# Kernel optimization log

Measured on AMD Instinct MI355X. Metric: run time of the kernel, lower is better.

The kernel has to match this reference:

```python
import jax, jax.numpy as jnp
import numpy as np

BLOCK = 100  # hard-coded block size in the original module


def setup_inputs() -> dict:
    key = jax.random.key(0)
    k1, k2 = jax.random.split(key)
    N_freqs = 128
    n = N_freqs * BLOCK  # 12800
    # DPP kernel: symmetric PD so every 100x100 diagonal block has positive logdet
    R = jax.random.normal(k1, (n, n), dtype=jnp.float32) * 0.05
    L_kernel = (R + R.T) * 0.5 + 2.0 * jnp.eye(n, dtype=jnp.float32)
    weights = jax.random.normal(k2, (n,), dtype=jnp.float32)
    return {"weights": weights, "L_kernel": L_kernel, "N_freqs": N_freqs}


def reference(weights, L_kernel, N_freqs):
    # Gather the N_freqs diagonal 100x100 blocks without touching off-diagonals
    blocks4 = L_kernel.reshape(N_freqs, BLOCK, N_freqs, BLOCK)
    idx = jnp.arange(N_freqs)
    diag_blocks = blocks4[idx, :, idx, :]  # [N_freqs, 100, 100]
    s = jax.nn.sigmoid(weights).reshape(N_freqs, BLOCK)  # [N_freqs, 100]
    I = jnp.eye(BLOCK, dtype=L_kernel.dtype)
    # diag(s_i) @ (B_i - I) + I, batched over blocks
    M = s[:, :, None] * (diag_blocks - I) + I  # [N_freqs, 100, 100]
    sign, logabs = jnp.linalg.slogdet(M)
    # torch.logdet returns nan for non-positive determinant
    logdets = jnp.where(sign > 0, logabs, jnp.nan)
    within_freq_dets = jnp.sum(logdets)
    within_freq_dets_tensor = logdets.astype(jnp.float32)
    return (within_freq_dets, within_freq_dets_tensor)
```

## Files before the change

### kernel.cpp

```cpp
#include <hip/hip_runtime.h>
#include <math.h>

#define BLK 100
#define NF  128
#define NTOT (NF * BLK)
#define P   104
#define NT  512

__device__ __forceinline__ float4 fnma4(float4 v, float s, const float4 p) {
    v.x -= s * p.x; v.y -= s * p.y; v.z -= s * p.z; v.w -= s * p.w; return v;
}
__device__ __forceinline__ float4 mul4(float4 v, float s) {
    v.x *= s; v.y *= s; v.z *= s; v.w *= s; return v;
}
__device__ __forceinline__ float rdl(float x, int l) {
    return __uint_as_float(__builtin_amdgcn_readlane(__float_as_uint(x), l));
}
__device__ __forceinline__ float4 swap32(float4 v) {
    float4 o;
    o.x = __shfl_xor(v.x, 32); o.y = __shfl_xor(v.y, 32);
    o.z = __shfl_xor(v.z, 32); o.w = __shfl_xor(v.w, 32);
    return o;
}

#define LD4(r, c4) (*reinterpret_cast<float4*>(&a[(r) * P + 4 * (c4)]))

#define PANEL_CORE()                                                           \
    {                                                                          \
        const float d0 = pp0.x, r0i = 1.0f / d0;                               \
        float l;                                                               \
        l = pp1.x * r0i;  pp1 = fnma4(pp1, l, pp0);  P1 = fnma4(P1, l, P0);    \
        const float d1 = pp1.y, r1i = 1.0f / d1;                               \
        l = pp2.x * r0i;  pp2 = fnma4(pp2, l, pp0);  P2 = fnma4(P2, l, P0);    \
        l = pp2.y * r1i;  pp2 = fnma4(pp2, l, pp1);  P2 = fnma4(P2, l, P1);    \
        const float d2 = pp2.z, r2i = 1.0f / d2;                               \
        l = pp3.x * r0i;  pp3 = fnma4(pp3, l, pp0);  P3 = fnma4(P3, l, P0);    \
        l = pp3.y * r1i;  pp3 = fnma4(pp3, l, pp1);  P3 = fnma4(P3, l, P1);    \
        l = pp3.z * r2i;  pp3 = fnma4(pp3, l, pp2);  P3 = fnma4(P3, l, P2);    \
        const float d3 = pp3.w, r3i = 1.0f / d3;                               \
        Q3 = mul4(P3, r3i);                                                    \
        Q2 = mul4(fnma4(P2, pp2.w, Q3), r2i);                                  \
        Q1 = mul4(fnma4(fnma4(P1, pp1.z, Q2), pp1.w, Q3), r1i);                \
        Q0 = mul4(fnma4(fnma4(fnma4(P0, pp0.y, Q1), pp0.z, Q2), pp0.w, Q3), r0i); \
        mant *= d0 * d1 * d2 * d3;                                             \
        { int t_; mant = frexpf(mant, &t_); e2 += t_; }                        \
        lneg += (d0 < 0.0f) + (d1 < 0.0f) + (d2 < 0.0f) + (d3 < 0.0f);         \
    }

#define SWEEP4(vv, pan)                                                        \
    vv = fnma4(vv, pan.x, Q0); vv = fnma4(vv, pan.y, Q1);                      \
    vv = fnma4(vv, pan.z, Q2); vv = fnma4(vv, pan.w, Q3);

__global__ __launch_bounds__(NT) void lu_logdet_kernel(const float* __restrict__ w,
                                                       const float* __restrict__ L,
                                                       float* __restrict__ out) {
    __shared__ float  a[BLK * P];
    __shared__ float4 qbuf[2][4][26];

    const int f    = blockIdx.x;
    const int tid  = threadIdx.x;
    const int wave = tid >> 6;
    const int sid  = tid >> 5;
    const int g    = tid & 31;
    const int gg   = (g < 25) ? g : 24;
    const int h    = sid & 1;

    const float* base = L + (size_t)f * BLK * NTOT + (size_t)f * BLK;
    for (int q = tid; q < BLK * 25; q += NT) {
        const int r  = q / 25;
        const int c0 = (q - r * 25) * 4;
        const float4 v = *reinterpret_cast<const float4*>(base + (size_t)r * NTOT + c0);
        const float sv = 1.0f / (1.0f + expf(-w[f * BLK + r]));
        const float ds = 1.0f - sv;
        float4 m;
        m.x = sv * v.x + ((c0 + 0) == r ? ds : 0.0f);
        m.y = sv * v.y + ((c0 + 1) == r ? ds : 0.0f);
        m.z = sv * v.z + ((c0 + 2) == r ? ds : 0.0f);
        m.w = sv * v.w + ((c0 + 3) == r ? ds : 0.0f);
        *reinterpret_cast<float4*>(&a[r * P + c0]) = m;
    }
    __syncthreads();

    float mant = 1.0f;
    int   e2   = 0;
    int   lneg = 0;
    float4 Q0, Q1, Q2, Q3;

    {
        float4 pp0 = LD4(0, 0), pp1 = LD4(1, 0), pp2 = LD4(2, 0), pp3 = LD4(3, 0);
        float4 P0 = LD4(0, gg), P1 = LD4(1, gg), P2 = LD4(2, gg), P3 = LD4(3, gg);
        PANEL_CORE()
    }

    for (int k0 = 0; k0 <= 92; k0 += 4) {
        const int gp = k0 >> 2;
        const int b  = gp & 1;
        const int nb = b ^ 1;

        if (wave == 0) {
            __builtin_amdgcn_s_setprio(1);
            const int i1 = k0 + 4 + h;
            const int i2 = k0 + 6 + h;
            const float4 pan1 = LD4(i1, gp);
            const float4 pan2 = LD4(i2, gp);
            float4 v1 = LD4(i1, gg);
            float4 v2 = LD4(i2, gg);
            SWEEP4(v1, pan1)
            SWEEP4(v2, pan2)
            const float4 o1 = swap32(v1);
            const float4 o2 = swap32(v2);
            float4 P0 = h ? o1 : v1;
            float4 P1 = h ? v1 : o1;
            float4 P2 = h ? o2 : v2;
            float4 P3 = h ? v2 : o2;
            const int gq = gp + 1;
            float4 pp0 = make_float4(rdl(P0.x, gq), rdl(P0.y, gq), rdl(P0.z, gq), rdl(P0.w, gq));
            float4 pp1 = make_float4(rdl(P1.x, gq), rdl(P1.y, gq), rdl(P1.z, gq), rdl(P1.w, gq));
            float4 pp2 = make_float4(rdl(P2.x, gq), rdl(P2.y, gq), rdl(P2.z, gq), rdl(P2.w, gq));
            float4 pp3 = make_float4(rdl(P3.x, gq), rdl(P3.y, gq), rdl(P3.z, gq), rdl(P3.w, gq));
            PANEL_CORE()
            if (g < 25) {
                qbuf[nb][0][g] = Q0; qbuf[nb][1][g] = Q1;
                qbuf[nb][2][g] = Q2; qbuf[nb][3][g] = Q3;
            }
            __builtin_amdgcn_s_setprio(0);
        } else {
            if (k0 > 0) {
                Q0 = qbuf[b][0][gg]; Q1 = qbuf[b][1][gg];
                Q2 = qbuf[b][2][gg]; Q3 = qbuf[b][3][gg];
            }
            if (g > gp && g < 25) {
                int i = k0 + 8 + (sid - 2);
                for (; i + 42 < BLK; i += 56) {
                    const float4 pa = LD4(i,      gp);
                    const float4 pb = LD4(i + 14, gp);
                    const float4 pc = LD4(i + 28, gp);
                    const float4 pd = LD4(i + 42, gp);
                    float4 va = LD4(i,      g);
                    float4 vb = LD4(i + 14, g);
                    float4 vc = LD4(i + 28, g);
                    float4 vd = LD4(i + 42, g);
                    SWEEP4(va, pa) SWEEP4(vb, pb) SWEEP4(vc, pc) SWEEP4(vd, pd)
                    LD4(i,      g) = va;
                    LD4(i + 14, g) = vb;
                    LD4(i + 28, g) = vc;
                    LD4(i + 42, g) = vd;
                }
                for (; i + 14 < BLK; i += 28) {
                    const float4 pa = LD4(i,      gp);
                    const float4 pb = LD4(i + 14, gp);
                    float4 va = LD4(i,      g);
                    float4 vb = LD4(i + 14, g);
                    SWEEP4(va, pa) SWEEP4(vb, pb)
                    LD4(i,      g) = va;
                    LD4(i + 14, g) = vb;
                }
                for (; i < BLK; i += 14) {
                    const float4 pa = LD4(i, gp);
                    float4 va = LD4(i, g);
                    SWEEP4(va, pa)
                    LD4(i, g) = va;
                }
            }
        }
        __syncthreads();
    }

    if (tid == 0) {
        float ld = logf(mant) + (float)e2 * 0.69314718055994531f;
        if ((lneg & 1) || !isfinite(ld)) ld = __int_as_float(0x7fc00000);
        out[1 + f] = ld;
        atomicAdd(out, ld);
    }
}

extern "C" void kernel_launch(void* const* d_in, const int* in_sizes, int n_in,
                              void* d_out, int out_size, void* d_ws, size_t ws_size,
                              hipStream_t stream) {
    const float* w = (const float*)d_in[0];
    const float* L = (const float*)d_in[1];
    float* out = (float*)d_out;
    hipMemsetAsync(d_out, 0, sizeof(float), stream);
    lu_logdet_kernel<<<NF, NT, 0, stream>>>(w, L, out);
}
```

Before: 31.79 us.

## Run final LU panels in a single wave without block barriers, use LDS panel loads

The wave-0 lookahead panel now writes its swept rows back to shared memory and reloads the 4x4 panel from LDS instead of using cross-half shuffles and readlane. The main loop stops earlier, and the last three panel steps run entirely inside wave 0 with no __syncthreads, since only a few column groups remain. This is meant to cut barrier and idle-wave overhead on the tail of the factorization, at the cost of serializing that tail on one wave and adding extra LDS traffic in the panel step.

```diff
diff --git a/kernel.cpp b/kernel.cpp
--- a/kernel.cpp
+++ b/kernel.cpp
@@ -13,20 +13,19 @@
 __device__ __forceinline__ float4 mul4(float4 v, float s) {
     v.x *= s; v.y *= s; v.z *= s; v.w *= s; return v;
 }
-__device__ __forceinline__ float rdl(float x, int l) {
-    return __uint_as_float(__builtin_amdgcn_readlane(__float_as_uint(x), l));
-}
-__device__ __forceinline__ float4 swap32(float4 v) {
-    float4 o;
-    o.x = __shfl_xor(v.x, 32); o.y = __shfl_xor(v.y, 32);
-    o.z = __shfl_xor(v.z, 32); o.w = __shfl_xor(v.w, 32);
-    return o;
-}
 
 #define LD4(r, c4) (*reinterpret_cast<float4*>(&a[(r) * P + 4 * (c4)]))
 
-#define PANEL_CORE()                                                           \
+#define PANEL_Q(kb, gq)                                                        \
     {                                                                          \
+        float4 pp0 = LD4((kb) + 0, (gq));                                      \
+        float4 pp1 = LD4((kb) + 1, (gq));                                      \
+        float4 pp2 = LD4((kb) + 2, (gq));                                      \
+        float4 pp3 = LD4((kb) + 3, (gq));                                      \
+        float4 P0  = LD4((kb) + 0, gg);                                        \
+        float4 P1  = LD4((kb) + 1, gg);                                        \
+        float4 P2  = LD4((kb) + 2, gg);                                        \
+        float4 P3  = LD4((kb) + 3, gg);                                        \
         const float d0 = pp0.x, r0i = 1.0f / d0;                               \
         float l;                                                               \
         l = pp1.x * r0i;  pp1 = fnma4(pp1, l, pp0);  P1 = fnma4(P1, l, P0);    \
@@ -86,39 +85,28 @@
     int   lneg = 0;
     float4 Q0, Q1, Q2, Q3;
 
-    {
-        float4 pp0 = LD4(0, 0), pp1 = LD4(1, 0), pp2 = LD4(2, 0), pp3 = LD4(3, 0);
-        float4 P0 = LD4(0, gg), P1 = LD4(1, gg), P2 = LD4(2, gg), P3 = LD4(3, gg);
-        PANEL_CORE()
-    }
-
-    for (int k0 = 0; k0 <= 92; k0 += 4) {
+    PANEL_Q(0, 0)
+
+    for (int k0 = 0; k0 <= 80; k0 += 4) {
         const int gp = k0 >> 2;
         const int b  = gp & 1;
         const int nb = b ^ 1;
 
         if (wave == 0) {
             __builtin_amdgcn_s_setprio(1);
-            const int i1 = k0 + 4 + h;
-            const int i2 = k0 + 6 + h;
-            const float4 pan1 = LD4(i1, gp);
-            const float4 pan2 = LD4(i2, gp);
-            float4 v1 = LD4(i1, gg);
-            float4 v2 = LD4(i2, gg);
-            SWEEP4(v1, pan1)
-            SWEEP4(v2, pan2)
-            const float4 o1 = swap32(v1);
-            const float4 o2 = swap32(v2);
-            float4 P0 = h ? o1 : v1;
-            float4 P1 = h ? v1 : o1;
-            float4 P2 = h ? o2 : v2;
-            float4 P3 = h ? v2 : o2;
-            const int gq = gp + 1;
-            float4 pp0 = make_float4(rdl(P0.x, gq), rdl(P0.y, gq), rdl(P0.z, gq), rdl(P0.w, gq));
-            float4 pp1 = make_float4(rdl(P1.x, gq), rdl(P1.y, gq), rdl(P1.z, gq), rdl(P1.w, gq));
-            float4 pp2 = make_float4(rdl(P2.x, gq), rdl(P2.y, gq), rdl(P2.z, gq), rdl(P2.w, gq));
-            float4 pp3 = make_float4(rdl(P3.x, gq), rdl(P3.y, gq), rdl(P3.z, gq), rdl(P3.w, gq));
-            PANEL_CORE()
+            if (g > gp && g < 25) {
+                const int i1 = k0 + 4 + h;
+                const int i2 = k0 + 6 + h;
+                const float4 pan1 = LD4(i1, gp);
+                const float4 pan2 = LD4(i2, gp);
+                float4 v1 = LD4(i1, g);
+                float4 v2 = LD4(i2, g);
+                SWEEP4(v1, pan1)
+                SWEEP4(v2, pan2)
+                LD4(i1, g) = v1;
+                LD4(i2, g) = v2;
+            }
+            PANEL_Q(k0 + 4, gp + 1)
             if (g < 25) {
                 qbuf[nb][0][g] = Q0; qbuf[nb][1][g] = Q1;
                 qbuf[nb][2][g] = Q2; qbuf[nb][3][g] = Q3;
@@ -166,6 +154,42 @@
         __syncthreads();
     }
 
+    if (wave == 0) {
+        if (g > 21 && g < 25) {
+            #pragma unroll
+            for (int j = 0; j < 6; ++j) {
+                const int r = 88 + 2 * j + h;
+                const float4 pan = LD4(r, 21);
+                float4 v = LD4(r, g);
+                SWEEP4(v, pan)
+                LD4(r, g) = v;
+            }
+        }
+        PANEL_Q(88, 22)
+        if (g > 22 && g < 25) {
+            #pragma unroll
+            for (int j = 0; j < 4; ++j) {
+                const int r = 92 + 2 * j + h;
+                const float4 pan = LD4(r, 22);
+                float4 v = LD4(r, g);
+                SWEEP4(v, pan)
+                LD4(r, g) = v;
+            }
+        }
+        PANEL_Q(92, 23)
+        if (g > 23 && g < 25) {
+            #pragma unroll
+            for (int j = 0; j < 2; ++j) {
+                const int r = 96 + 2 * j + h;
+                const float4 pan = LD4(r, 23);
+                float4 v = LD4(r, g);
+                SWEEP4(v, pan)
+                LD4(r, g) = v;
+            }
+        }
+        PANEL_Q(96, 24)
+    }
+
     if (tid == 0) {
         float ld = logf(mant) + (float)e2 * 0.69314718055994531f;
         if ((lneg & 1) || !isfinite(ld)) ld = __int_as_float(0x7fc00000);
```

Result: faster. 30.32 us (-4.6%).
